# Optimization experiments

Hardware: AMD Instinct MI355X
Metric: run time of the kernel (lower is better)

## Reference

```python
import jax, jax.numpy as jnp
import numpy as np

N, F, D = 32, 1024, 512
H = 2 * D  # dim * ratio
EPS = 1e-5


def batchnorm1d(x, gamma, beta):
    # x: (N, F, L); BatchNorm1d over channel dim F, stats over (N, L) (training mode, biased var)
    mean = jnp.mean(x, axis=(0, 2), keepdims=True)
    var = jnp.var(x, axis=(0, 2), keepdims=True)
    xn = (x - mean) * jax.lax.rsqrt(var + EPS)
    return xn * gamma[None, :, None] + beta[None, :, None]


def setup_inputs() -> dict:
    key = jax.random.key(0)
    ks = jax.random.split(key, 5)
    x = jax.random.normal(ks[0], (N, F, D), dtype=jnp.float32)
    W0 = jax.random.normal(ks[1], (H, D), dtype=jnp.float32) * 0.02  # Linear(D->H) weight (out,in)
    b0 = jnp.zeros((H,), jnp.float32)
    W1 = jax.random.normal(ks[2], (D, H), dtype=jnp.float32) * 0.02  # Linear(H->D)
    b1 = jnp.zeros((D,), jnp.float32)
    Wc = jax.random.normal(ks[3], (F, F), dtype=jnp.float32) * 0.02  # Conv1d k=1 weight (out_ch,in_ch)
    bc = jnp.zeros((F,), jnp.float32)
    ones = jnp.ones((F,), jnp.float32)
    zeros = jnp.zeros((F,), jnp.float32)
    return {
        "x": x,
        "W0": W0, "b0": b0, "g0": ones, "be0": zeros,
        "W1": W1, "b1": b1, "g1": ones, "be1": zeros,
        "gf": ones, "bf": zeros,
        "Wc": Wc, "bc": bc,
        "go": ones, "bo": zeros,
    }


def reference(x, W0, b0, g0, be0, W1, b1, g1, be1, gf, bf, Wc, bc, go, bo):
    # proj_mlp0: Linear(D->H) + BN1d(F)
    v = jnp.einsum('nfd,hd->nfh', x, W0) + b0  # (N, F, H)
    v = batchnorm1d(v, g0, be0)
    # correlation: bmm(v, v^T) -> softsign -> bmm(w, v)
    w = jnp.einsum('nfh,ngh->nfg', v, v)  # (N, F, F)
    w = w / (1.0 + jnp.abs(w))  # softsign
    v = jnp.einsum('nfg,ngh->nfh', w, v)  # (N, F, H)
    # proj_mlp1: Linear(H->D) + BN1d(F)
    v = jnp.einsum('nfh,dh->nfd', v, W1) + b1  # (N, F, D)
    v = batchnorm1d(v, g1, be1)
    # feed_norm(v + x)
    xr = batchnorm1d(v + x, gf, bf)
    # proj_conv: Conv1d(F->F, kernel=1) over channel dim
    v = jnp.einsum('oi,nid->nod', Wc, xr) + bc[None, :, None]
    return batchnorm1d(v + xr, go, bo)
```

## Files before the change

kernel.cpp:

```cpp
#include <hip/hip_runtime.h>
#include <stdint.h>

#define NB 32
#define FC 1024
#define DD 512
#define HH 1024
#define BN_EPS 1e-5f

typedef unsigned short u16;
typedef unsigned int u32;
typedef __attribute__((ext_vector_type(8))) short bf16x8;
typedef __attribute__((ext_vector_type(4))) float f32x4;
typedef __attribute__((ext_vector_type(8))) unsigned short ushort8v;

#define AS1 __attribute__((address_space(1)))
#define AS3 __attribute__((address_space(3)))

__device__ __forceinline__ float b2f(u16 u) {
    union { u32 i; float f; } v;
    v.i = ((u32)u) << 16;
    return v.f;
}
__device__ __forceinline__ u16 f2b(float f) {
    union { float f; u32 i; } v;
    v.f = f;
    const u32 b = v.i;
    return (u16)((b + 0x7FFFu + ((b >> 16) & 1u)) >> 16);
}

__device__ __forceinline__ void gld16(const u16* g, u16* l) {
    __builtin_amdgcn_global_load_lds((const AS1 u32*)g, (AS3 u32*)l, 16, 0, 0);
}

__device__ __forceinline__ void swizzle_tiles(int& mt, int& nt, int& zt) {
    const int gx = gridDim.x, gy = gridDim.y, gz = gridDim.z;
    const int mzTot = gy * gz;
    if ((mzTot & 7) != 0) { nt = blockIdx.x; mt = blockIdx.y; zt = blockIdx.z; return; }
    long lin = ((long)blockIdx.z * gy + blockIdx.y) * gx + blockIdx.x;
    const int slab = mzTot >> 3;
    const int xcd = (int)(lin & 7);
    const long idx = lin >> 3;
    nt = (int)(idx % gx);
    const int mz = (int)(idx / gx) + xcd * slab;
    mt = mz % gy;
    zt = mz / gy;
}

__global__ __launch_bounds__(256) void detect_dtype(
    const u32* __restrict__ x, int* __restrict__ flag)
{
    __shared__ int cnt[256];
    int c = 0;
    for (int i = threadIdx.x; i < 4096; i += 256) {
        const u32 lo = x[i] & 0xFFFFu;
        const u32 e = (lo >> 7) & 0xFFu;
        if (e >= 0x68u && e <= 0x85u) c++;
    }
    cnt[threadIdx.x] = c;
    __syncthreads();
    for (int s = 128; s > 0; s >>= 1) {
        if (threadIdx.x < (unsigned)s) cnt[threadIdx.x] += cnt[threadIdx.x + s];
        __syncthreads();
    }
    if (threadIdx.x == 0) flag[0] = (cnt[0] > 2048) ? 1 : 0;
}

__global__ __launch_bounds__(256) void convert_to_bf16(
    const void* __restrict__ src, u16* __restrict__ dst, long n4,
    const int* __restrict__ flag)
{
    const bool isbf = (*flag != 0);
    long i4 = (long)blockIdx.x * blockDim.x + threadIdx.x;
    const long stride = (long)gridDim.x * blockDim.x;
    for (; i4 < n4; i4 += stride) {
        const long i = i4 << 2;
        if (isbf) {
            *(ushort4*)(dst + i) = *(const ushort4*)((const u16*)src + i);
        } else {
            const float4 v = *(const float4*)((const float*)src + i);
            ushort4 o;
            o.x = f2b(v.x); o.y = f2b(v.y); o.z = f2b(v.z); o.w = f2b(v.w);
            *(ushort4*)(dst + i) = o;
        }
    }
}

template<bool BIAS, bool SOFTSIGN>
__global__ __launch_bounds__(512, 2) void gemm256_nt(
    const u16* __restrict__ A, const u16* __restrict__ B,
    const u16* __restrict__ bias, u16* __restrict__ C,
    int M, int N, int K, int lda, int ldb, int ldc,
    long sA, long sB, long sC)
{
    extern __shared__ char smem[];

    int mt, nt, zt;
    swizzle_tiles(mt, nt, zt);
    const u16* Ab = A + (long)zt * sA + (long)(mt * 256) * lda;
    const u16* Bb = B + (long)zt * sB + (long)(nt * 256) * ldb;
    C += (long)zt * sC;

    const int tid  = threadIdx.x;
    const int lane = tid & 63;
    const int wv   = tid >> 6;
    const int wr   = (wv >> 2) * 128;
    const int wc   = (wv & 3) * 64;
    const int lm   = lane & 15;
    const int q    = lane >> 4;

    int aOff[2][4], bOff[4];
    #pragma unroll
    for (int mh = 0; mh < 2; ++mh)
        #pragma unroll
        for (int i = 0; i < 4; ++i) {
            const int r = wr + mh * 64 + i * 16 + lm;
            aOff[mh][i] = r * 64 + ((q ^ ((r >> 1) & 3)) << 4);
        }
    #pragma unroll
    for (int j = 0; j < 4; ++j) {
        const int r = wc + j * 16 + lm;
        bOff[j] = r * 64 + ((q ^ ((r >> 1) & 3)) << 4);
    }

    const int rw = lane >> 2, qs = lane & 3;
    const u16* pA[2]; const u16* pB[2];
    int ldsC[2];
    #pragma unroll
    for (int c = 0; c < 2; ++c) {
        const int r = wv * 32 + c * 16 + rw;
        const int kq = (qs ^ ((r >> 1) & 3)) << 3;
        pA[c] = Ab + (long)r * lda + kq;
        pB[c] = Bb + (long)r * ldb + kq;
        ldsC[c] = wv * 2048 + c * 1024;
    }

#define STAGE(bufOff, kofs) { \
    gld16(pA[0] + (kofs), (u16*)(smem + (bufOff) + ldsC[0])); \
    gld16(pA[1] + (kofs), (u16*)(smem + (bufOff) + ldsC[1])); \
    gld16(pB[0] + (kofs), (u16*)(smem + (bufOff) + 16384 + ldsC[0])); \
    gld16(pB[1] + (kofs), (u16*)(smem + (bufOff) + 16384 + ldsC[1])); }

#define RDA(mh, bo) { \
    const char* base_ = smem + (bo); \
    a[0] = *(const bf16x8*)(base_ + aOff[mh][0]); \
    a[1] = *(const bf16x8*)(base_ + aOff[mh][1]); \
    a[2] = *(const bf16x8*)(base_ + aOff[mh][2]); \
    a[3] = *(const bf16x8*)(base_ + aOff[mh][3]); }

#define RDB(bo) { \
    const char* base_ = smem + (bo) + 16384; \
    b[0] = *(const bf16x8*)(base_ + bOff[0]); \
    b[1] = *(const bf16x8*)(base_ + bOff[1]); \
    b[2] = *(const bf16x8*)(base_ + bOff[2]); \
    b[3] = *(const bf16x8*)(base_ + bOff[3]); }

#define MMA(mh) do { \
    __builtin_amdgcn_s_setprio(1); \
    acc[(mh)*4+0][0] = __builtin_amdgcn_mfma_f32_16x16x32_bf16(a[0], b[0], acc[(mh)*4+0][0], 0,0,0); \
    acc[(mh)*4+0][1] = __builtin_amdgcn_mfma_f32_16x16x32_bf16(a[0], b[1], acc[(mh)*4+0][1], 0,0,0); \
    acc[(mh)*4+0][2] = __builtin_amdgcn_mfma_f32_16x16x32_bf16(a[0], b[2], acc[(mh)*4+0][2], 0,0,0); \
    acc[(mh)*4+0][3] = __builtin_amdgcn_mfma_f32_16x16x32_bf16(a[0], b[3], acc[(mh)*4+0][3], 0,0,0); \
    acc[(mh)*4+1][0] = __builtin_amdgcn_mfma_f32_16x16x32_bf16(a[1], b[0], acc[(mh)*4+1][0], 0,0,0); \
    acc[(mh)*4+1][1] = __builtin_amdgcn_mfma_f32_16x16x32_bf16(a[1], b[1], acc[(mh)*4+1][1], 0,0,0); \
    acc[(mh)*4+1][2] = __builtin_amdgcn_mfma_f32_16x16x32_bf16(a[1], b[2], acc[(mh)*4+1][2], 0,0,0); \
    acc[(mh)*4+1][3] = __builtin_amdgcn_mfma_f32_16x16x32_bf16(a[1], b[3], acc[(mh)*4+1][3], 0,0,0); \
    acc[(mh)*4+2][0] = __builtin_amdgcn_mfma_f32_16x16x32_bf16(a[2], b[0], acc[(mh)*4+2][0], 0,0,0); \
    acc[(mh)*4+2][1] = __builtin_amdgcn_mfma_f32_16x16x32_bf16(a[2], b[1], acc[(mh)*4+2][1], 0,0,0); \
    acc[(mh)*4+2][2] = __builtin_amdgcn_mfma_f32_16x16x32_bf16(a[2], b[2], acc[(mh)*4+2][2], 0,0,0); \
    acc[(mh)*4+2][3] = __builtin_amdgcn_mfma_f32_16x16x32_bf16(a[2], b[3], acc[(mh)*4+2][3], 0,0,0); \
    acc[(mh)*4+3][0] = __builtin_amdgcn_mfma_f32_16x16x32_bf16(a[3], b[0], acc[(mh)*4+3][0], 0,0,0); \
    acc[(mh)*4+3][1] = __builtin_amdgcn_mfma_f32_16x16x32_bf16(a[3], b[1], acc[(mh)*4+3][1], 0,0,0); \
    acc[(mh)*4+3][2] = __builtin_amdgcn_mfma_f32_16x16x32_bf16(a[3], b[2], acc[(mh)*4+3][2], 0,0,0); \
    acc[(mh)*4+3][3] = __builtin_amdgcn_mfma_f32_16x16x32_bf16(a[3], b[3], acc[(mh)*4+3][3], 0,0,0); \
    __builtin_amdgcn_s_setprio(0); \
} while (0)

#define BAR() __builtin_amdgcn_s_barrier()
#define WAIT_VM8() { asm volatile("s_waitcnt vmcnt(8)" ::: "memory"); \
                     __builtin_amdgcn_sched_barrier(0); }

    f32x4 acc[8][4] = {};
    bf16x8 a[4], b[4];

    const int NT = K >> 5;

    STAGE(0, 0);
    STAGE(32768, 32);
    STAGE(65536, 64);
    WAIT_VM8();
    BAR();

    for (int t = 0; t < NT; ++t) {
        const int bo = (t & 3) * 32768;
        const int bn = ((t + 3) & 3) * 32768;
        const int kn = ((t + 3 < NT) ? (t + 3) : (NT - 1)) * 32;

        RDA(0, bo); RDB(bo);
        STAGE(bn, kn);
        BAR(); MMA(0); BAR();
        RDA(1, bo);
        WAIT_VM8();
        BAR(); MMA(1); BAR();
    }

#undef STAGE
#undef RDA
#undef RDB
#undef MMA
#undef BAR
#undef WAIT_VM8

    asm volatile("s_waitcnt vmcnt(0)" ::: "memory");
    __builtin_amdgcn_sched_barrier(0);
    __syncthreads();

    float* rep = (float*)smem + wv * (16 * 65);
    const int rr = lane >> 2;
    const int cg = lane & 3;
    const int m0 = mt * 256;
    const int n0 = nt * 256;
    #pragma unroll
    for (int i = 0; i < 8; ++i) {
        #pragma unroll
        for (int j = 0; j < 4; ++j) {
            const int col = 16 * j + lm;
            const float bj = BIAS ? b2f(bias[n0 + wc + col]) : 0.0f;
            #pragma unroll
            for (int r = 0; r < 4; ++r) {
                float v = acc[i][j][r] + bj;
                if (SOFTSIGN) v = v / (1.0f + fabsf(v));
                rep[(q * 4 + r) * 65 + col] = v;
            }
        }
        const float* lr = rep + rr * 65 + cg * 16;
        const float4 f0 = *(const float4*)(lr + 0);
        const float4 f1 = *(const float4*)(lr + 4);
        const float4 f2 = *(const float4*)(lr + 8);
        const float4 f3 = *(const float4*)(lr + 12);
        ushort8v o0, o1;
        o0[0] = f2b(f0.x); o0[1] = f2b(f0.y); o0[2] = f2b(f0.z); o0[3] = f2b(f0.w);
        o0[4] = f2b(f1.x); o0[5] = f2b(f1.y); o0[6] = f2b(f1.z); o0[7] = f2b(f1.w);
        o1[0] = f2b(f2.x); o1[1] = f2b(f2.y); o1[2] = f2b(f2.z); o1[3] = f2b(f2.w);
        o1[4] = f2b(f3.x); o1[5] = f2b(f3.y); o1[6] = f2b(f3.z); o1[7] = f2b(f3.w);
        u16* cp = C + (long)(m0 + wr + 16 * i + rr) * ldc + n0 + wc + cg * 16;
        *(ushort8v*)cp = o0;
        *(ushort8v*)(cp + 8) = o1;
    }
}

__global__ __launch_bounds__(256) void transpose_bf16(
    const u16* __restrict__ src, u16* __restrict__ dst,
    int R, int Cc, long sS, long sD)
{
    __shared__ u16 t[32][33];
    const int bz = blockIdx.z;
    src += (long)bz * sS;
    dst += (long)bz * sD;
    const int c0 = blockIdx.x * 32;
    const int r0 = blockIdx.y * 32;
    const int lx = threadIdx.x & 31;
    const int ly = threadIdx.x >> 5;
    #pragma unroll
    for (int d = 0; d < 32; d += 8)
        t[ly + d][lx] = src[(long)(r0 + ly + d) * Cc + c0 + lx];
    __syncthreads();
    #pragma unroll
    for (int d = 0; d < 32; d += 8)
        dst[(long)(c0 + ly + d) * R + r0 + lx] = t[lx][ly + d];
}

__global__ __launch_bounds__(256) void bn_stats(
    const u16* __restrict__ src, const u16* __restrict__ gamma,
    const u16* __restrict__ beta, float* __restrict__ ss,
    int Lc, int nOuter)
{
    const int f = blockIdx.x;
    const long outerStride = (long)FC * Lc;
    const u16* base = src + (long)f * Lc;

    const int vecs = Lc >> 2;
    const int tpn  = (vecs < 256) ? vecs : 256;
    const int nGrp = 256 / tpn;
    const int sub  = threadIdx.x / tpn;
    const int off4 = (threadIdx.x % tpn) << 2;

    float s1 = 0.f, s2 = 0.f;
    for (int n = sub; n < nOuter; n += nGrp) {
        const u16* p = base + (long)n * outerStride;
        for (int i = off4; i < Lc; i += (tpn << 2)) {
            const ushort4 v = *(const ushort4*)(p + i);
            const float a = b2f(v.x), b = b2f(v.y), c = b2f(v.z), d = b2f(v.w);
            s1 += a + b + c + d;
            s2 += a * a + b * b + c * c + d * d;
        }
    }

    __shared__ float r1[256], r2[256];
    const int tid = threadIdx.x;
    r1[tid] = s1;
    r2[tid] = s2;
    __syncthreads();
    for (int s = 128; s > 0; s >>= 1) {
        if (tid < s) { r1[tid] += r1[tid + s]; r2[tid] += r2[tid + s]; }
        __syncthreads();
    }
    if (tid == 0) {
        const float cnt  = (float)nOuter * (float)Lc;
        const float mean = r1[0] / cnt;
        const float var  = r2[0] / cnt - mean * mean;
        const float rstd = rsqrtf(var + BN_EPS);
        const float sc   = b2f(gamma[f]) * rstd;
        ss[f]      = sc;
        ss[FC + f] = b2f(beta[f]) - mean * sc;
    }
}

template<bool ADD>
__global__ __launch_bounds__(256) void bn_apply(
    const u16* __restrict__ src, const void* __restrict__ add,
    const int* __restrict__ addflag,
    const float* __restrict__ ss, void* __restrict__ dst,
    const int* __restrict__ outflag, long total4, int lcShift)
{
    const bool addf32 = ADD && (addflag != nullptr) && (*addflag == 0);
    const bool outf32 = (outflag != nullptr) && (*outflag == 0);
    long i4 = (long)blockIdx.x * blockDim.x + threadIdx.x;
    const long stride = (long)gridDim.x * blockDim.x;
    for (; i4 < total4; i4 += stride) {
        const long i = i4 << 2;
        const int c = (int)((i >> lcShift) & (FC - 1));
        const float sc = ss[c];
        const float sh = ss[FC + c];
        const ushort4 v = *(const ushort4*)(src + i);
        float o0 = fmaf(b2f(v.x), sc, sh);
        float o1 = fmaf(b2f(v.y), sc, sh);
        float o2 = fmaf(b2f(v.z), sc, sh);
        float o3 = fmaf(b2f(v.w), sc, sh);
        if (ADD) {
            if (addf32) {
                const float4 a = *(const float4*)((const float*)add + i);
                o0 += a.x; o1 += a.y; o2 += a.z; o3 += a.w;
            } else {
                const ushort4 a = *(const ushort4*)((const u16*)add + i);
                o0 += b2f(a.x); o1 += b2f(a.y); o2 += b2f(a.z); o3 += b2f(a.w);
            }
        }
        if (outf32) {
            float4 o; o.x = o0; o.y = o1; o.z = o2; o.w = o3;
            *(float4*)((float*)dst + i) = o;
        } else {
            ushort4 o;
            o.x = f2b(o0); o.y = f2b(o1); o.z = f2b(o2); o.w = f2b(o3);
            *(ushort4*)((u16*)dst + i) = o;
        }
    }
}

__global__ __launch_bounds__(256) void add3_bias(
    const u16* __restrict__ a, const u16* __restrict__ b,
    const u16* __restrict__ bias, u16* __restrict__ dst,
    long total4, int lcShift)
{
    long i4 = (long)blockIdx.x * blockDim.x + threadIdx.x;
    const long stride = (long)gridDim.x * blockDim.x;
    for (; i4 < total4; i4 += stride) {
        const long i = i4 << 2;
        const int c = (int)((i >> lcShift) & (FC - 1));
        const float bs = b2f(bias[c]);
        const ushort4 va = *(const ushort4*)(a + i);
        const ushort4 vb = *(const ushort4*)(b + i);
        ushort4 o;
        o.x = f2b(b2f(va.x) + b2f(vb.x) + bs);
        o.y = f2b(b2f(va.y) + b2f(vb.y) + bs);
        o.z = f2b(b2f(va.z) + b2f(vb.z) + bs);
        o.w = f2b(b2f(va.w) + b2f(vb.w) + bs);
        *(ushort4*)(dst + i) = o;
    }
}

extern "C" void kernel_launch(void* const* d_in, const int* in_sizes, int n_in,
                              void* d_out, int out_size, void* d_ws, size_t ws_size,
                              hipStream_t stream)
{
    const size_t MiB = (size_t)1 << 20;
    const long sFH = (long)FC * HH;
    const long sFF = (long)FC * FC;
    const long sFD = (long)FC * DD;
    const long VE  = (long)NB * FC * HH;
    const long PE  = (long)NB * FC * DD;

    const size_t GLDS = 131072;
    static bool s_attr = false;
    if (!s_attr) {
        s_attr = true;
        hipFuncSetAttribute(reinterpret_cast<const void*>(&gemm256_nt<true, false>),
                            hipFuncAttributeMaxDynamicSharedMemorySize, (int)GLDS);
        hipFuncSetAttribute(reinterpret_cast<const void*>(&gemm256_nt<false, true>),
                            hipFuncAttributeMaxDynamicSharedMemorySize, (int)GLDS);
        hipFuncSetAttribute(reinterpret_cast<const void*>(&gemm256_nt<false, false>),
                            hipFuncAttributeMaxDynamicSharedMemorySize, (int)GLDS);
    }

    long off[16];
    long cur = 0;
    for (int i = 1; i < 15; ++i) { off[i] = cur; cur += ((long)in_sizes[i] + 7) & ~7L; }
    const size_t paramBytes = (size_t)cur * 2;

    int cb = 16;
    while (cb > 1 &&
           64 * MiB + (size_t)cb * 6 * MiB + paramBytes + 16384 > ws_size)
        cb >>= 1;

    u16* V   = (u16*)d_ws;
    u16* VT  = (u16*)((char*)d_ws + 64 * MiB);
    u16* WW  = VT + (long)cb * sFH;
    u16* V2  = WW + (long)cb * sFF;
    u16* WC  = V2 + (long)cb * sFH;
    char* tail = (char*)(WC + cur);
    tail = (char*)(((uintptr_t)tail + 255) & ~(uintptr_t)255);
    float* SS   = (float*)tail;
    int*   FLAG = (int*)(SS + 2 * FC);
    u16* VX  = (u16*)d_out;
    u16* XB  = (u16*)d_out + PE;
    u16* V4  = V;
    u16* XRT = V + PE;

    const dim3 blk(256);
    const dim3 blk512(512);
    const dim3 egrid(4096);

    detect_dtype<<<1, blk, 0, stream>>>((const u32*)d_in[0], FLAG);
    for (int i = 1; i < 15; ++i) {
        const long n4 = (long)in_sizes[i] / 4;
        int g = (int)((n4 + 255) / 256);
        if (g > 1024) g = 1024;
        if (g < 1) g = 1;
        convert_to_bf16<<<dim3(g), blk, 0, stream>>>(d_in[i], WC + off[i], n4, FLAG);
    }
    convert_to_bf16<<<dim3(1024), blk, 0, stream>>>(d_in[0], XB, PE / 4, FLAG);

    const u16* W0c = WC + off[1];
    const u16* b0c = WC + off[2];
    const u16* g0c = WC + off[3];
    const u16* be0c = WC + off[4];
    const u16* W1c = WC + off[5];
    const u16* b1c = WC + off[6];
    const u16* g1c = WC + off[7];
    const u16* be1c = WC + off[8];
    const u16* gfc = WC + off[9];
    const u16* bfc = WC + off[10];
    const u16* Wcc = WC + off[11];
    const u16* bcc = WC + off[12];
    const u16* goc = WC + off[13];
    const u16* boc = WC + off[14];

    gemm256_nt<true, false><<<dim3(HH / 256, (NB * FC) / 256, 1), blk512, GLDS, stream>>>(
        XB, W0c, b0c, V, NB * FC, HH, DD, DD, DD, HH, 0, 0, 0);

    bn_stats<<<FC, blk, 0, stream>>>(V, g0c, be0c, SS, HH, NB);
    bn_apply<false><<<egrid, blk, 0, stream>>>(V, nullptr, nullptr, SS, V, nullptr, VE / 4, 10);

    for (int bz0 = 0; bz0 < NB; bz0 += cb) {
        const int c = (NB - bz0 < cb) ? (NB - bz0) : cb;
        transpose_bf16<<<dim3(HH / 32, FC / 32, c), blk, 0, stream>>>(
            V + bz0 * sFH, VT, FC, HH, sFH, sFH);
        gemm256_nt<false, true><<<dim3(FC / 256, FC / 256, c), blk512, GLDS, stream>>>(
            V + bz0 * sFH, V + bz0 * sFH, nullptr, WW,
            FC, FC, HH, HH, HH, FC, sFH, sFH, sFF);
        gemm256_nt<false, false><<<dim3(HH / 256, FC / 256, c), blk512, GLDS, stream>>>(
            WW, VT, nullptr, V2,
            FC, HH, FC, FC, FC, HH, sFF, sFH, sFH);
        gemm256_nt<true, false><<<dim3(DD / 256, (c * FC) / 256, 1), blk512, GLDS, stream>>>(
            V2, W1c, b1c, VX + bz0 * sFD,
            c * FC, DD, HH, HH, HH, DD, 0, 0, 0);
    }

    bn_stats<<<FC, blk, 0, stream>>>(VX, g1c, be1c, SS, DD, NB);
    bn_apply<true><<<egrid, blk, 0, stream>>>(VX, XB, nullptr, SS, VX, nullptr, PE / 4, 9);

    bn_stats<<<FC, blk, 0, stream>>>(VX, gfc, bfc, SS, DD, NB);
    bn_apply<false><<<egrid, blk, 0, stream>>>(VX, nullptr, nullptr, SS, VX, nullptr, PE / 4, 9);

    transpose_bf16<<<dim3(DD / 32, FC / 32, NB), blk, 0, stream>>>(
        VX, XRT, FC, DD, sFD, sFD);
    gemm256_nt<false, false><<<dim3(DD / 256, FC / 256, NB), blk512, GLDS, stream>>>(
        Wcc, XRT, nullptr, V4, FC, DD, FC, FC, FC, DD, 0, sFD, sFD);

    add3_bias<<<egrid, blk, 0, stream>>>(V4, VX, bcc, V4, PE / 4, 9);

    bn_stats<<<FC, blk, 0, stream>>>(V4, goc, boc, SS, DD, NB);
    bn_apply<false><<<egrid, blk, 0, stream>>>(V4, nullptr, nullptr, SS, d_out, FLAG, PE / 4, 9);
}
```

Before: 690.3 us.

## Shrink GEMM tile to 128x256 with simple double-buffered pipeline

Replaces the 256x256 GEMM tile with a 128x256 tile and halves the accumulator count. The 4-stage LDS pipeline with its manual waitcnt and barrier choreography becomes a plain 2-stage double buffer synchronised with __syncthreads. LDS drops from 128KB to 48KB and launch bounds allow 4 blocks per CU, aiming for higher occupancy and more tiles in flight. The correlation batch chunk doubles to 32. In exchange the kernel loses data reuse per tile and the deeper prefetch, so it may expose more memory latency.

New measurement: 671.4 us. 1.03x faster.

```diff
diff --git a/kernel.cpp b/kernel.cpp
--- a/kernel.cpp
+++ b/kernel.cpp
@@ -86,7 +86,7 @@
 }
 
 template<bool BIAS, bool SOFTSIGN>
-__global__ __launch_bounds__(512, 2) void gemm256_nt(
+__global__ __launch_bounds__(512, 4) void gemm128x256_nt(
     const u16* __restrict__ A, const u16* __restrict__ B,
     const u16* __restrict__ bias, u16* __restrict__ C,
     int M, int N, int K, int lda, int ldb, int ldc,
@@ -96,26 +96,24 @@
 
     int mt, nt, zt;
     swizzle_tiles(mt, nt, zt);
-    const u16* Ab = A + (long)zt * sA + (long)(mt * 256) * lda;
+    const u16* Ab = A + (long)zt * sA + (long)(mt * 128) * lda;
     const u16* Bb = B + (long)zt * sB + (long)(nt * 256) * ldb;
     C += (long)zt * sC;
 
     const int tid  = threadIdx.x;
     const int lane = tid & 63;
     const int wv   = tid >> 6;
-    const int wr   = (wv >> 2) * 128;
+    const int wrr  = (wv >> 2) * 64;
     const int wc   = (wv & 3) * 64;
     const int lm   = lane & 15;
     const int q    = lane >> 4;
 
-    int aOff[2][4], bOff[4];
+    int aOff[4], bOff[4];
     #pragma unroll
-    for (int mh = 0; mh < 2; ++mh)
-        #pragma unroll
-        for (int i = 0; i < 4; ++i) {
-            const int r = wr + mh * 64 + i * 16 + lm;
-            aOff[mh][i] = r * 64 + ((q ^ ((r >> 1) & 3)) << 4);
-        }
+    for (int i = 0; i < 4; ++i) {
+        const int r = wrr + i * 16 + lm;
+        aOff[i] = r * 64 + ((q ^ ((r >> 1) & 3)) << 4);
+    }
     #pragma unroll
     for (int j = 0; j < 4; ++j) {
         const int r = wc + j * 16 + lm;
@@ -123,104 +121,60 @@
     }
 
     const int rw = lane >> 2, qs = lane & 3;
-    const u16* pA[2]; const u16* pB[2];
-    int ldsC[2];
-    #pragma unroll
-    for (int c = 0; c < 2; ++c) {
-        const int r = wv * 32 + c * 16 + rw;
-        const int kq = (qs ^ ((r >> 1) & 3)) << 3;
-        pA[c] = Ab + (long)r * lda + kq;
-        pB[c] = Bb + (long)r * ldb + kq;
-        ldsC[c] = wv * 2048 + c * 1024;
-    }
+    const int rA  = wv * 16 + rw;
+    const int rB0 = wv * 32 + rw;
+    const int rB1 = wv * 32 + 16 + rw;
+    const u16* pA  = Ab + (long)rA  * lda + ((qs ^ ((rA  >> 1) & 3)) << 3);
+    const u16* pB0 = Bb + (long)rB0 * ldb + ((qs ^ ((rB0 >> 1) & 3)) << 3);
+    const u16* pB1 = Bb + (long)rB1 * ldb + ((qs ^ ((rB1 >> 1) & 3)) << 3);
+    const int ldsA  = wv * 1024;
+    const int ldsB0 = wv * 2048;
+    const int ldsB1 = wv * 2048 + 1024;
 
 #define STAGE(bufOff, kofs) { \
-    gld16(pA[0] + (kofs), (u16*)(smem + (bufOff) + ldsC[0])); \
-    gld16(pA[1] + (kofs), (u16*)(smem + (bufOff) + ldsC[1])); \
-    gld16(pB[0] + (kofs), (u16*)(smem + (bufOff) + 16384 + ldsC[0])); \
-    gld16(pB[1] + (kofs), (u16*)(smem + (bufOff) + 16384 + ldsC[1])); }
-
-#define RDA(mh, bo) { \
-    const char* base_ = smem + (bo); \
-    a[0] = *(const bf16x8*)(base_ + aOff[mh][0]); \
-    a[1] = *(const bf16x8*)(base_ + aOff[mh][1]); \
-    a[2] = *(const bf16x8*)(base_ + aOff[mh][2]); \
-    a[3] = *(const bf16x8*)(base_ + aOff[mh][3]); }
-
-#define RDB(bo) { \
-    const char* base_ = smem + (bo) + 16384; \
-    b[0] = *(const bf16x8*)(base_ + bOff[0]); \
-    b[1] = *(const bf16x8*)(base_ + bOff[1]); \
-    b[2] = *(const bf16x8*)(base_ + bOff[2]); \
-    b[3] = *(const bf16x8*)(base_ + bOff[3]); }
-
-#define MMA(mh) do { \
-    __builtin_amdgcn_s_setprio(1); \
-    acc[(mh)*4+0][0] = __builtin_amdgcn_mfma_f32_16x16x32_bf16(a[0], b[0], acc[(mh)*4+0][0], 0,0,0); \
-    acc[(mh)*4+0][1] = __builtin_amdgcn_mfma_f32_16x16x32_bf16(a[0], b[1], acc[(mh)*4+0][1], 0,0,0); \
-    acc[(mh)*4+0][2] = __builtin_amdgcn_mfma_f32_16x16x32_bf16(a[0], b[2], acc[(mh)*4+0][2], 0,0,0); \
-    acc[(mh)*4+0][3] = __builtin_amdgcn_mfma_f32_16x16x32_bf16(a[0], b[3], acc[(mh)*4+0][3], 0,0,0); \
-    acc[(mh)*4+1][0] = __builtin_amdgcn_mfma_f32_16x16x32_bf16(a[1], b[0], acc[(mh)*4+1][0], 0,0,0); \
-    acc[(mh)*4+1][1] = __builtin_amdgcn_mfma_f32_16x16x32_bf16(a[1], b[1], acc[(mh)*4+1][1], 0,0,0); \
-    acc[(mh)*4+1][2] = __builtin_amdgcn_mfma_f32_16x16x32_bf16(a[1], b[2], acc[(mh)*4+1][2], 0,0,0); \
-    acc[(mh)*4+1][3] = __builtin_amdgcn_mfma_f32_16x16x32_bf16(a[1], b[3], acc[(mh)*4+1][3], 0,0,0); \
-    acc[(mh)*4+2][0] = __builtin_amdgcn_mfma_f32_16x16x32_bf16(a[2], b[0], acc[(mh)*4+2][0], 0,0,0); \
-    acc[(mh)*4+2][1] = __builtin_amdgcn_mfma_f32_16x16x32_bf16(a[2], b[1], acc[(mh)*4+2][1], 0,0,0); \
-    acc[(mh)*4+2][2] = __builtin_amdgcn_mfma_f32_16x16x32_bf16(a[2], b[2], acc[(mh)*4+2][2], 0,0,0); \
-    acc[(mh)*4+2][3] = __builtin_amdgcn_mfma_f32_16x16x32_bf16(a[2], b[3], acc[(mh)*4+2][3], 0,0,0); \
-    acc[(mh)*4+3][0] = __builtin_amdgcn_mfma_f32_16x16x32_bf16(a[3], b[0], acc[(mh)*4+3][0], 0,0,0); \
-    acc[(mh)*4+3][1] = __builtin_amdgcn_mfma_f32_16x16x32_bf16(a[3], b[1], acc[(mh)*4+3][1], 0,0,0); \
-    acc[(mh)*4+3][2] = __builtin_amdgcn_mfma_f32_16x16x32_bf16(a[3], b[2], acc[(mh)*4+3][2], 0,0,0); \
-    acc[(mh)*4+3][3] = __builtin_amdgcn_mfma_f32_16x16x32_bf16(a[3], b[3], acc[(mh)*4+3][3], 0,0,0); \
-    __builtin_amdgcn_s_setprio(0); \
-} while (0)
-
-#define BAR() __builtin_amdgcn_s_barrier()
-#define WAIT_VM8() { asm volatile("s_waitcnt vmcnt(8)" ::: "memory"); \
-                     __builtin_amdgcn_sched_barrier(0); }
-
-    f32x4 acc[8][4] = {};
-    bf16x8 a[4], b[4];
+    gld16(pA  + (kofs), (u16*)(smem + (bufOff) + ldsA)); \
+    gld16(pB0 + (kofs), (u16*)(smem + (bufOff) + 8192 + ldsB0)); \
+    gld16(pB1 + (kofs), (u16*)(smem + (bufOff) + 8192 + ldsB1)); }
+
+    f32x4 acc[4][4] = {};
 
     const int NT = K >> 5;
 
     STAGE(0, 0);
-    STAGE(32768, 32);
-    STAGE(65536, 64);
-    WAIT_VM8();
-    BAR();
+    __syncthreads();
 
     for (int t = 0; t < NT; ++t) {
-        const int bo = (t & 3) * 32768;
-        const int bn = ((t + 3) & 3) * 32768;
-        const int kn = ((t + 3 < NT) ? (t + 3) : (NT - 1)) * 32;
-
-        RDA(0, bo); RDB(bo);
-        STAGE(bn, kn);
-        BAR(); MMA(0); BAR();
-        RDA(1, bo);
-        WAIT_VM8();
-        BAR(); MMA(1); BAR();
+        const int bo = (t & 1) * 24576;
+        const int bn = ((t + 1) & 1) * 24576;
+        if (t + 1 < NT) STAGE(bn, (t + 1) * 32);
+
+        bf16x8 a[4], b[4];
+        const char* baseA = smem + bo;
+        const char* baseB = smem + bo + 8192;
+        #pragma unroll
+        for (int i = 0; i < 4; ++i) a[i] = *(const bf16x8*)(baseA + aOff[i]);
+        #pragma unroll
+        for (int j = 0; j < 4; ++j) b[j] = *(const bf16x8*)(baseB + bOff[j]);
+
+        #pragma unroll
+        for (int i = 0; i < 4; ++i)
+            #pragma unroll
+            for (int j = 0; j < 4; ++j)
+                acc[i][j] = __builtin_amdgcn_mfma_f32_16x16x32_bf16(
+                    a[i], b[j], acc[i][j], 0, 0, 0);
+
+        __syncthreads();
     }
 
 #undef STAGE
-#undef RDA
-#undef RDB
-#undef MMA
-#undef BAR
-#undef WAIT_VM8
-
-    asm volatile("s_waitcnt vmcnt(0)" ::: "memory");
-    __builtin_amdgcn_sched_barrier(0);
-    __syncthreads();
 
     float* rep = (float*)smem + wv * (16 * 65);
     const int rr = lane >> 2;
     const int cg = lane & 3;
-    const int m0 = mt * 256;
+    const int m0 = mt * 128;
     const int n0 = nt * 256;
     #pragma unroll
-    for (int i = 0; i < 8; ++i) {
+    for (int i = 0; i < 4; ++i) {
         #pragma unroll
         for (int j = 0; j < 4; ++j) {
             const int col = 16 * j + lm;
@@ -242,7 +196,7 @@
         o0[4] = f2b(f1.x); o0[5] = f2b(f1.y); o0[6] = f2b(f1.z); o0[7] = f2b(f1.w);
         o1[0] = f2b(f2.x); o1[1] = f2b(f2.y); o1[2] = f2b(f2.z); o1[3] = f2b(f2.w);
         o1[4] = f2b(f3.x); o1[5] = f2b(f3.y); o1[6] = f2b(f3.z); o1[7] = f2b(f3.w);
-        u16* cp = C + (long)(m0 + wr + 16 * i + rr) * ldc + n0 + wc + cg * 16;
+        u16* cp = C + (long)(m0 + wrr + 16 * i + rr) * ldc + n0 + wc + cg * 16;
         *(ushort8v*)cp = o0;
         *(ushort8v*)(cp + 8) = o1;
     }
@@ -389,15 +343,15 @@
     const long VE  = (long)NB * FC * HH;
     const long PE  = (long)NB * FC * DD;
 
-    const size_t GLDS = 131072;
+    const size_t GLDS = 49152;
     static bool s_attr = false;
     if (!s_attr) {
         s_attr = true;
-        hipFuncSetAttribute(reinterpret_cast<const void*>(&gemm256_nt<true, false>),
+        hipFuncSetAttribute(reinterpret_cast<const void*>(&gemm128x256_nt<true, false>),
                             hipFuncAttributeMaxDynamicSharedMemorySize, (int)GLDS);
-        hipFuncSetAttribute(reinterpret_cast<const void*>(&gemm256_nt<false, true>),
+        hipFuncSetAttribute(reinterpret_cast<const void*>(&gemm128x256_nt<false, true>),
                             hipFuncAttributeMaxDynamicSharedMemorySize, (int)GLDS);
-        hipFuncSetAttribute(reinterpret_cast<const void*>(&gemm256_nt<false, false>),
+        hipFuncSetAttribute(reinterpret_cast<const void*>(&gemm128x256_nt<false, false>),
                             hipFuncAttributeMaxDynamicSharedMemorySize, (int)GLDS);
     }
 
@@ -406,7 +360,7 @@
     for (int i = 1; i < 15; ++i) { off[i] = cur; cur += ((long)in_sizes[i] + 7) & ~7L; }
     const size_t paramBytes = (size_t)cur * 2;
 
-    int cb = 16;
+    int cb = 32;
     while (cb > 1 &&
            64 * MiB + (size_t)cb * 6 * MiB + paramBytes + 16384 > ws_size)
         cb >>= 1;
@@ -454,7 +408,7 @@
     const u16* goc = WC + off[13];
     const u16* boc = WC + off[14];
 
-    gemm256_nt<true, false><<<dim3(HH / 256, (NB * FC) / 256, 1), blk512, GLDS, stream>>>(
+    gemm128x256_nt<true, false><<<dim3(HH / 256, (NB * FC) / 128, 1), blk512, GLDS, stream>>>(
         XB, W0c, b0c, V, NB * FC, HH, DD, DD, DD, HH, 0, 0, 0);
 
     bn_stats<<<FC, blk, 0, stream>>>(V, g0c, be0c, SS, HH, NB);
@@ -464,13 +418,13 @@
         const int c = (NB - bz0 < cb) ? (NB - bz0) : cb;
         transpose_bf16<<<dim3(HH / 32, FC / 32, c), blk, 0, stream>>>(
             V + bz0 * sFH, VT, FC, HH, sFH, sFH);
-        gemm256_nt<false, true><<<dim3(FC / 256, FC / 256, c), blk512, GLDS, stream>>>(
+        gemm128x256_nt<false, true><<<dim3(FC / 256, FC / 128, c), blk512, GLDS, stream>>>(
             V + bz0 * sFH, V + bz0 * sFH, nullptr, WW,
             FC, FC, HH, HH, HH, FC, sFH, sFH, sFF);
-        gemm256_nt<false, false><<<dim3(HH / 256, FC / 256, c), blk512, GLDS, stream>>>(
+        gemm128x256_nt<false, false><<<dim3(HH / 256, FC / 128, c), blk512, GLDS, stream>>>(
             WW, VT, nullptr, V2,
             FC, HH, FC, FC, FC, HH, sFF, sFH, sFH);
-        gemm256_nt<true, false><<<dim3(DD / 256, (c * FC) / 256, 1), blk512, GLDS, stream>>>(
+        gemm128x256_nt<true, false><<<dim3(DD / 256, (c * FC) / 128, 1), blk512, GLDS, stream>>>(
             V2, W1c, b1c, VX + bz0 * sFD,
             c * FC, DD, HH, HH, HH, DD, 0, 0, 0);
     }
@@ -483,7 +437,7 @@
 
     transpose_bf16<<<dim3(DD / 32, FC / 32, NB), blk, 0, stream>>>(
         VX, XRT, FC, DD, sFD, sFD);
-    gemm256_nt<false, false><<<dim3(DD / 256, FC / 256, NB), blk512, GLDS, stream>>>(
+    gemm128x256_nt<false, false><<<dim3(DD / 256, FC / 128, NB), blk512, GLDS, stream>>>(
         Wcc, XRT, nullptr, V4, FC, DD, FC, FC, FC, DD, 0, sFD, sFD);
 
     add3_bias<<<egrid, blk, 0, stream>>>(V4, VX, bcc, V4, PE / 4, 9);
```
